# Kernel tuning notes

Hardware: AMD Instinct MI355X
Metric: run time of the kernel (lower is better)

The kernel has to match this reference:

```python
import jax, jax.numpy as jnp
import numpy as np

D_MODEL = 2048
NUM_HEADS = 32
NUM_KV_HEADS = 8
DIM_HEAD = D_MODEL // NUM_HEADS  # 64
REPS = NUM_HEADS // NUM_KV_HEADS  # 4
B, T = 2, 2048


def setup_inputs() -> dict:
    key = jax.random.key(0)
    k_x, k_q, k_k, k_v, k_o = jax.random.split(key, 5)
    s = 1.0 / np.sqrt(D_MODEL)
    return {
        "x": jax.random.normal(k_x, (B, T, D_MODEL), dtype=jnp.float32),
        "wq": jax.random.normal(k_q, (D_MODEL, NUM_HEADS * DIM_HEAD), dtype=jnp.float32) * s,
        "wk": jax.random.normal(k_k, (D_MODEL, NUM_KV_HEADS * DIM_HEAD), dtype=jnp.float32) * s,
        "wv": jax.random.normal(k_v, (D_MODEL, NUM_KV_HEADS * DIM_HEAD), dtype=jnp.float32) * s,
        "wo": jax.random.normal(k_o, (D_MODEL, D_MODEL), dtype=jnp.float32) * s,
    }


def reference(x, wq, wk, wv, wo):
    Bb, Tt, _ = x.shape
    q = (x @ wq).reshape(Bb, Tt, NUM_HEADS, DIM_HEAD)       # [B,T,H,dh]
    k = (x @ wk).reshape(Bb, Tt, NUM_KV_HEADS, DIM_HEAD)    # [B,T,Hkv,dh]
    v = (x @ wv).reshape(Bb, Tt, NUM_KV_HEADS, DIM_HEAD)
    # repeat_interleave KV heads to match Q heads
    k = jnp.repeat(k, REPS, axis=2)                          # [B,T,H,dh]
    v = jnp.repeat(v, REPS, axis=2)
    scale = 1.0 / np.sqrt(DIM_HEAD).astype(np.float32)
    scores = jnp.einsum('bqhd,bkhd->bhqk', q, k) * scale     # [B,H,T,T]
    causal = jnp.tril(jnp.ones((Tt, Tt), dtype=bool))
    scores = jnp.where(causal, scores, -jnp.inf)
    attn = jax.nn.softmax(scores, axis=-1)
    out = jnp.einsum('bhqk,bkhd->bqhd', attn, v)             # [B,T,H,dh]
    out = out.reshape(Bb, Tt, NUM_HEADS * DIM_HEAD)
    return out @ wo
```

## Files before the change

kernel.cpp:

```cpp
#include <hip/hip_runtime.h>

typedef unsigned short u16;
typedef unsigned int u32;
typedef unsigned long long u64;

typedef __bf16 bf16x8 __attribute__((ext_vector_type(8)));
typedef float f32x4 __attribute__((ext_vector_type(4)));
typedef float f32x16 __attribute__((ext_vector_type(16)));
typedef u16 u16x4 __attribute__((ext_vector_type(4)));
typedef u32 u32x4v __attribute__((ext_vector_type(4)));

__device__ __forceinline__ u16 f2bf(float f) {
  u32 u = __builtin_bit_cast(u32, f);
  u += 0x7fffu + ((u >> 16) & 1u);
  return (u16)(u >> 16);
}

__device__ __forceinline__ u32 packbf2(float a, float b) {
  __bf16 x = (__bf16)a, y = (__bf16)b;
  return (u32)__builtin_bit_cast(u16, x) | ((u32)__builtin_bit_cast(u16, y) << 16);
}

__device__ __forceinline__ float fexp2(float x) {
#if __has_builtin(__builtin_amdgcn_exp2f)
  return __builtin_amdgcn_exp2f(x);
#else
  return exp2f(x);
#endif
}

__device__ __forceinline__ void gload_lds16(const void* g, void* lds) {
  __builtin_amdgcn_global_load_lds(
      (const __attribute__((address_space(1))) void*)g,
      (__attribute__((address_space(3))) void*)lds, 16, 0, 0);
}

#define QSCALE 0.18033688011112043f

__global__ __launch_bounds__(256) void prep_kernel(
    const float* __restrict__ x, u16* __restrict__ xb,
    const float* __restrict__ wq, const float* __restrict__ wk,
    const float* __restrict__ wv, const float* __restrict__ wo,
    u16* __restrict__ wqT, u16* __restrict__ wkT,
    u16* __restrict__ wvT, u16* __restrict__ woT) {
  __shared__ float tile[32][33];
  int bid = blockIdx.x;
  if (bid < 8192) {
    int i = (bid * 256 + threadIdx.x) * 4;
    float4 v = *reinterpret_cast<const float4*>(x + i);
    u16x4 o;
    o[0] = f2bf(v.x); o[1] = f2bf(v.y); o[2] = f2bf(v.z); o[3] = f2bf(v.w);
    *reinterpret_cast<u16x4*>(xb + i) = o;
    return;
  }
  bid -= 8192;
  constexpr int K = 2048;
  const float* w_;
  u16* wt;
  int N;
  switch (bid >> 12) {
    case 0: w_ = wq; wt = wqT; N = 2048; break;
    case 1: w_ = wo; wt = woT; N = 2048; break;
    case 2: w_ = wk; wt = wkT; N = 512; break;
    default: w_ = wv; wt = wvT; N = 512; break;
  }
  int rem = bid & 4095;
  int bx = (rem & 63) * 32;
  if (bx >= N) return;
  int by = (rem >> 6) * 32;
  int tx = threadIdx.x & 31, ty = threadIdx.x >> 5;
#pragma unroll
  for (int i = 0; i < 32; i += 8)
    tile[ty + i][tx] = w_[(size_t)(by + ty + i) * N + bx + tx];
  __syncthreads();
#pragma unroll
  for (int i = 0; i < 32; i += 8)
    wt[(size_t)(bx + ty + i) * K + by + tx] = f2bf(tile[tx][ty + i]);
}

__global__ __launch_bounds__(512, 1) void gemm_qkv(
    const u16* __restrict__ A, const u16* __restrict__ BT,
    u16* __restrict__ Cb, u16* __restrict__ Cb2, u16* __restrict__ Cb3) {
  constexpr int K = 2048, NT = 32;
  __shared__ __align__(16) u16 Ab[2][256 * 64];
  __shared__ __align__(16) u16 Bb[2][192 * 64];
  const int t = threadIdx.x;
  const int lane = t & 63;
  const int w = t >> 6;
  const int wm = w >> 2, wn = w & 3;
  const int l15 = lane & 15, l4 = lane >> 4;

  const int nwg = gridDim.x * gridDim.y;
  const int bid = blockIdx.y * gridDim.x + blockIdx.x;
  const int wg = (bid & 7) * (nwg >> 3) + (bid >> 3);
  const int brow = (wg / gridDim.x) * 256;
  const int bcol = (wg % gridDim.x) * 192;

  const int r0 = t >> 3;
  const int gc = ((t & 7) ^ (r0 & 7)) * 8;
  auto stageA = [&](int q, int h, int kt) {
    const u16* src = A + (size_t)(brow + h * 128 + r0) * K + kt * 64 + gc;
    u16* dst = &Ab[q][(h * 128 + r0) * 64 + (t & 7) * 8];
    gload_lds16(src, dst);
    gload_lds16(src + (size_t)64 * K, dst + 64 * 64);
  };
  auto stageB = [&](int q, int c, int kt) {
    const u16* src = BT + (size_t)(bcol + c * 64 + r0) * K + kt * 64 + gc;
    u16* dst = &Bb[q][(c * 64 + r0) * 64 + (t & 7) * 8];
    gload_lds16(src, dst);
  };

  f32x4 acc[8][3];
#pragma unroll
  for (int mi = 0; mi < 8; mi++)
#pragma unroll
    for (int n = 0; n < 3; n++)
#pragma unroll
      for (int r = 0; r < 4; r++) acc[mi][n][r] = 0.f;

  stageA(0, 0, 0); stageA(0, 1, 0);
  stageB(0, 0, 0); stageB(0, 1, 0); stageB(0, 2, 0);
  stageA(1, 0, 1); stageA(1, 1, 1);
  asm volatile("s_waitcnt vmcnt(4)" ::: "memory");
  __builtin_amdgcn_sched_barrier(0);
  __builtin_amdgcn_s_barrier();

  for (int kt = 0; kt < NT; ++kt) {
    const int q = kt & 1;
    const u16* Al = Ab[q];
    const u16* Bl = Bb[q];
    bf16x8 af[8][2], bf[3][2];

#pragma unroll
    for (int m = 0; m < 4; ++m) {
      int row = wm * 128 + m * 16 + l15;
#pragma unroll
      for (int ks = 0; ks < 2; ++ks)
        af[m][ks] = *reinterpret_cast<const bf16x8*>(
            &Al[row * 64 + (((ks * 4 + l4) ^ (row & 7)) * 8)]);
    }
#pragma unroll
    for (int n = 0; n < 3; ++n) {
      int row = wn * 48 + n * 16 + l15;
#pragma unroll
      for (int ks = 0; ks < 2; ++ks)
        bf[n][ks] = *reinterpret_cast<const bf16x8*>(
            &Bl[row * 64 + (((ks * 4 + l4) ^ (row & 7)) * 8)]);
    }
    if (kt + 1 < NT) stageB(q ^ 1, 0, kt + 1);
    __builtin_amdgcn_s_barrier();
    __builtin_amdgcn_s_setprio(1);
#pragma unroll
    for (int ks = 0; ks < 2; ++ks)
#pragma unroll
      for (int m = 0; m < 4; ++m)
#pragma unroll
        for (int n = 0; n < 2; ++n)
          acc[m][n] = __builtin_amdgcn_mfma_f32_16x16x32_bf16(
              af[m][ks], bf[n][ks], acc[m][n], 0, 0, 0);
    __builtin_amdgcn_s_setprio(0);
    __builtin_amdgcn_s_barrier();

#pragma unroll
    for (int m = 4; m < 8; ++m) {
      int row = wm * 128 + m * 16 + l15;
#pragma unroll
      for (int ks = 0; ks < 2; ++ks)
        af[m][ks] = *reinterpret_cast<const bf16x8*>(
            &Al[row * 64 + (((ks * 4 + l4) ^ (row & 7)) * 8)]);
    }
    if (kt + 1 < NT) { stageB(q ^ 1, 1, kt + 1); stageB(q ^ 1, 2, kt + 1); }
    __builtin_amdgcn_s_barrier();
    __builtin_amdgcn_s_setprio(1);
#pragma unroll
    for (int ks = 0; ks < 2; ++ks)
#pragma unroll
      for (int m = 0; m < 4; ++m)
        acc[m][2] = __builtin_amdgcn_mfma_f32_16x16x32_bf16(
            af[m][ks], bf[2][ks], acc[m][2], 0, 0, 0);
    __builtin_amdgcn_s_setprio(0);
    __builtin_amdgcn_s_barrier();

    if (kt + 2 < NT) stageA(q, 0, kt + 2);
    __builtin_amdgcn_s_barrier();
    __builtin_amdgcn_s_setprio(1);
#pragma unroll
    for (int ks = 0; ks < 2; ++ks)
#pragma unroll
      for (int m = 4; m < 8; ++m)
#pragma unroll
        for (int n = 0; n < 2; ++n)
          acc[m][n] = __builtin_amdgcn_mfma_f32_16x16x32_bf16(
              af[m][ks], bf[n][ks], acc[m][n], 0, 0, 0);
    __builtin_amdgcn_s_setprio(0);
    __builtin_amdgcn_s_barrier();

    if (kt + 2 < NT) stageA(q, 1, kt + 2);
    __builtin_amdgcn_s_barrier();
    __builtin_amdgcn_s_setprio(1);
#pragma unroll
    for (int ks = 0; ks < 2; ++ks)
#pragma unroll
      for (int m = 4; m < 8; ++m)
        acc[m][2] = __builtin_amdgcn_mfma_f32_16x16x32_bf16(
            af[m][ks], bf[2][ks], acc[m][2], 0, 0, 0);
    __builtin_amdgcn_s_setprio(0);
    if (kt + 2 < NT) {
      asm volatile("s_waitcnt vmcnt(4)" ::: "memory");
    } else {
      asm volatile("s_waitcnt vmcnt(0)" ::: "memory");
    }
    __builtin_amdgcn_sched_barrier(0);
    __builtin_amdgcn_s_barrier();
  }

#pragma unroll
  for (int mi = 0; mi < 8; ++mi) {
    int grow0 = brow + wm * 128 + mi * 16 + l4 * 4;
#pragma unroll
    for (int n = 0; n < 3; ++n) {
      int gbase = bcol + wn * 48 + n * 16;
      int gcol = gbase + l15;
      if (gbase < 2048) {
#pragma unroll
        for (int r = 0; r < 4; ++r)
          Cb[(size_t)(grow0 + r) * 2048 + gcol] = f2bf(acc[mi][n][r] * QSCALE);
      } else if (gbase < 2560) {
#pragma unroll
        for (int r = 0; r < 4; ++r)
          Cb2[(size_t)(grow0 + r) * 512 + (gcol - 2048)] = f2bf(acc[mi][n][r]);
      } else {
        int col = gcol - 2560;
        int bb = grow0 >> 11, tt = grow0 & 2047;
        u64 wv = (u64)packbf2(acc[mi][n][0], acc[mi][n][1]) |
                 ((u64)packbf2(acc[mi][n][2], acc[mi][n][3]) << 32);
        *reinterpret_cast<u64*>(&Cb3[((size_t)(bb * 512 + col)) * 2048 + tt]) = wv;
      }
    }
  }
}

__global__ __launch_bounds__(512, 2) void gemm256n(
    const u16* __restrict__ A, const u16* __restrict__ BT,
    float* __restrict__ Cf, int M, int N) {
  constexpr int K = 2048, NT = 32;
  __shared__ __align__(16) u16 Ab[2][256 * 64];
  __shared__ __align__(16) u16 Bb[2][128 * 64];
  const int t = threadIdx.x;
  const int lane = t & 63;
  const int w = t >> 6;
  const int wm = w >> 1, wn = w & 1;
  const int l15 = lane & 15, l4 = lane >> 4;

  const int nwg = gridDim.x * gridDim.y;
  const int bid = blockIdx.y * gridDim.x + blockIdx.x;
  const int wg = (bid & 7) * (nwg >> 3) + (bid >> 3);
  const int brow = (wg / gridDim.x) * 256;
  const int bcol = (wg % gridDim.x) * 128;

  const int r0 = t >> 3;
  const int gc = ((t & 7) ^ (r0 & 7)) * 8;
  auto stageA = [&](int q, int h, int kt) {
    const u16* src = A + (size_t)(brow + h * 128 + r0) * K + kt * 64 + gc;
    u16* dst = &Ab[q][(h * 128 + r0) * 64 + (t & 7) * 8];
    gload_lds16(src, dst);
    gload_lds16(src + (size_t)64 * K, dst + 64 * 64);
  };
  auto stageB = [&](int q, int h, int kt) {
    const u16* src = BT + (size_t)(bcol + h * 64 + r0) * K + kt * 64 + gc;
    u16* dst = &Bb[q][(h * 64 + r0) * 64 + (t & 7) * 8];
    gload_lds16(src, dst);
  };

  f32x4 acc[4][4];
#pragma unroll
  for (int m = 0; m < 4; m++)
#pragma unroll
    for (int n = 0; n < 4; n++)
#pragma unroll
      for (int r = 0; r < 4; r++) acc[m][n][r] = 0.f;

  stageA(0, 0, 0); stageA(0, 1, 0);
  stageB(0, 0, 0); stageB(0, 1, 0);
  stageA(1, 0, 1); stageA(1, 1, 1);
  asm volatile("s_waitcnt vmcnt(4)" ::: "memory");
  __builtin_amdgcn_sched_barrier(0);
  __builtin_amdgcn_s_barrier();

  for (int kt = 0; kt < NT; ++kt) {
    const int q = kt & 1;
    const u16* Al = Ab[q];
    const u16* Bl = Bb[q];
    bf16x8 af[4][2], bf[4][2];

#pragma unroll
    for (int m = 0; m < 2; ++m) {
      int row = wm * 64 + m * 16 + l15;
#pragma unroll
      for (int ks = 0; ks < 2; ++ks)
        af[m][ks] = *reinterpret_cast<const bf16x8*>(
            &Al[row * 64 + (((ks * 4 + l4) ^ (row & 7)) * 8)]);
    }
#pragma unroll
    for (int n = 0; n < 2; ++n) {
      int row = wn * 64 + n * 16 + l15;
#pragma unroll
      for (int ks = 0; ks < 2; ++ks)
        bf[n][ks] = *reinterpret_cast<const bf16x8*>(
            &Bl[row * 64 + (((ks * 4 + l4) ^ (row & 7)) * 8)]);
    }
    if (kt + 1 < NT) stageB(q ^ 1, 0, kt + 1);
    __builtin_amdgcn_s_barrier();
    __builtin_amdgcn_s_setprio(1);
#pragma unroll
    for (int ks = 0; ks < 2; ++ks)
#pragma unroll
      for (int m = 0; m < 2; ++m)
#pragma unroll
        for (int n = 0; n < 2; ++n)
          acc[m][n] = __builtin_amdgcn_mfma_f32_16x16x32_bf16(
              af[m][ks], bf[n][ks], acc[m][n], 0, 0, 0);
    __builtin_amdgcn_s_setprio(0);
    __builtin_amdgcn_s_barrier();

#pragma unroll
    for (int m = 2; m < 4; ++m) {
      int row = wm * 64 + m * 16 + l15;
#pragma unroll
      for (int ks = 0; ks < 2; ++ks)
        af[m][ks] = *reinterpret_cast<const bf16x8*>(
            &Al[row * 64 + (((ks * 4 + l4) ^ (row & 7)) * 8)]);
    }
#pragma unroll
    for (int n = 2; n < 4; ++n) {
      int row = wn * 64 + n * 16 + l15;
#pragma unroll
      for (int ks = 0; ks < 2; ++ks)
        bf[n][ks] = *reinterpret_cast<const bf16x8*>(
            &Bl[row * 64 + (((ks * 4 + l4) ^ (row & 7)) * 8)]);
    }
    if (kt + 1 < NT) stageB(q ^ 1, 1, kt + 1);
    __builtin_amdgcn_s_barrier();
    __builtin_amdgcn_s_setprio(1);
#pragma unroll
    for (int ks = 0; ks < 2; ++ks)
#pragma unroll
      for (int m = 0; m < 2; ++m)
#pragma unroll
        for (int n = 2; n < 4; ++n)
          acc[m][n] = __builtin_amdgcn_mfma_f32_16x16x32_bf16(
              af[m][ks], bf[n][ks], acc[m][n], 0, 0, 0);
    __builtin_amdgcn_s_setprio(0);
    __builtin_amdgcn_s_barrier();

    if (kt + 2 < NT) stageA(q, 0, kt + 2);
    __builtin_amdgcn_s_barrier();
    __builtin_amdgcn_s_setprio(1);
#pragma unroll
    for (int ks = 0; ks < 2; ++ks)
#pragma unroll
      for (int m = 2; m < 4; ++m)
#pragma unroll
        for (int n = 0; n < 2; ++n)
          acc[m][n] = __builtin_amdgcn_mfma_f32_16x16x32_bf16(
              af[m][ks], bf[n][ks], acc[m][n], 0, 0, 0);
    __builtin_amdgcn_s_setprio(0);
    __builtin_amdgcn_s_barrier();

    if (kt + 2 < NT) stageA(q, 1, kt + 2);
    __builtin_amdgcn_s_barrier();
    __builtin_amdgcn_s_setprio(1);
#pragma unroll
    for (int ks = 0; ks < 2; ++ks)
#pragma unroll
      for (int m = 2; m < 4; ++m)
#pragma unroll
        for (int n = 2; n < 4; ++n)
          acc[m][n] = __builtin_amdgcn_mfma_f32_16x16x32_bf16(
              af[m][ks], bf[n][ks], acc[m][n], 0, 0, 0);
    __builtin_amdgcn_s_setprio(0);
    if (kt + 2 < NT) {
      asm volatile("s_waitcnt vmcnt(4)" ::: "memory");
    } else {
      asm volatile("s_waitcnt vmcnt(0)" ::: "memory");
    }
    __builtin_amdgcn_sched_barrier(0);
    __builtin_amdgcn_s_barrier();
  }

#pragma unroll
  for (int m = 0; m < 4; ++m) {
    int grow0 = brow + wm * 64 + m * 16 + l4 * 4;
#pragma unroll
    for (int n = 0; n < 4; ++n) {
      int gcol = bcol + wn * 64 + n * 16 + l15;
#pragma unroll
      for (int r = 0; r < 4; ++r)
        Cf[(size_t)(grow0 + r) * N + gcol] = acc[m][n][r];
    }
  }
}

__global__ __launch_bounds__(256, 2) void attn_kernel(
    const u16* __restrict__ Qb, const u16* __restrict__ Kb,
    const u16* __restrict__ VT, u16* __restrict__ Ob) {
  const int bx = blockIdx.x;
  const int kvh = bx & 7;
  const int u = bx >> 3;
  const int jj = u & 7;
  const int v = u >> 3;
  const int h = kvh * 4 + (v & 3);
  const int b = v >> 2;
  const int t = threadIdx.x;
  const int lane = t & 63;
  const int w = t >> 6;
  const int q31 = lane & 31;
  const int hi = lane >> 5;

  __shared__ __align__(16) u16 Ks[2][64 * 64];
  __shared__ __align__(16) u16 Vs[2][64 * 64];
  __shared__ __align__(16) u32 Po[4][32 * 32];

  const size_t Krow0 = (size_t)b * 2048;
  const size_t Vrow0 = ((size_t)b * 8 + kvh) * 64;

  u16* const dk0 = &Ks[0][t * 8];
  u16* const dk1 = &Ks[1][t * 8];
  u16* const dv0 = &Vs[0][t * 8];
  u16* const dv1 = &Vs[1][t * 8];
  const int row0 = t >> 3;
  const int gcs = ((t & 7) ^ (row0 & 7)) * 8;
  const u16* const pk0 = Kb + (Krow0 + row0) * 512 + kvh * 64 + gcs;
  const u16* const pv0 = VT + (Vrow0 + row0) * 2048 + gcs;
  const u16* kp = pk0;
  const u16* vp = pv0;

  auto stage = [&](int buf, const u16* kpp, const u16* vpp) {
    u16* dk = buf ? dk1 : dk0;
    u16* dv = buf ? dv1 : dv0;
    gload_lds16(kpp, dk);
    gload_lds16(kpp + 32 * 512, dk + 2048);
    gload_lds16(vpp, dv);
    gload_lds16(vpp + 32 * 2048, dv + 2048);
  };

  const int swk = (q31 & 7);
  const int nA = 2 * (15 - jj) + 2;
  const int nsteps = 34;

  stage(0, kp, vp);
  __syncthreads();
  int cur = 0;
  int ss = 0;

#pragma unroll
  for (int ph = 0; ph < 2; ++ph) {
    const int qt = ph ? jj : 15 - jj;
    const int nkv = 2 * qt + 2;
    const int wq0 = qt * 128 + w * 32;
    const int mylast = (wq0 + 31) >> 6;

    bf16x8 qf[4];
    {
      const u16* q0 = &Qb[((size_t)b * 2048 + wq0 + q31) * 2048 + h * 64 + hi * 8];
      qf[0] = *reinterpret_cast<const bf16x8*>(q0);
      qf[1] = *reinterpret_cast<const bf16x8*>(q0 + 16);
      qf[2] = *reinterpret_cast<const bf16x8*>(q0 + 32);
      qf[3] = *reinterpret_cast<const bf16x8*>(q0 + 48);
    }

    f32x16 oo0, oo1;
#pragma unroll
    for (int r = 0; r < 16; ++r) { oo0[r] = 0.f; oo1[r] = 0.f; }
    float mr = -1e30f, lr = 0.f;

    for (int kv = 0; kv < nkv; ++kv, ++ss) {
      const int kvbase = kv << 6;
      if (ss + 1 < nsteps) {
        if (ss + 1 == nA) {
          kp = pk0;
          vp = pv0;
        } else {
          kp += 64 * 512;
          vp += 64;
        }
        stage(cur ^ 1, kp, vp);
      }

      if (kv <= mylast) {
        f32x16 s0, s1;
#pragma unroll
        for (int r = 0; r < 16; ++r) { s0[r] = 0.f; s1[r] = 0.f; }
        __builtin_amdgcn_s_setprio(1);
#pragma unroll
        for (int kc = 0; kc < 4; ++kc) {
          const int kcol = ((kc * 2 + hi) ^ swk) * 8;
          bf16x8 kb0 = *reinterpret_cast<const bf16x8*>(&Ks[cur][q31 * 64 + kcol]);
          bf16x8 kb1 = *reinterpret_cast<const bf16x8*>(&Ks[cur][(32 + q31) * 64 + kcol]);
          s0 = __builtin_amdgcn_mfma_f32_32x32x16_bf16(kb0, qf[kc], s0, 0, 0, 0);
          s1 = __builtin_amdgcn_mfma_f32_32x32x16_bf16(kb1, qf[kc], s1, 0, 0, 0);
        }
        __builtin_amdgcn_s_setprio(0);

        if (kvbase + 63 > wq0) {
          const int qg = wq0 + q31;
#pragma unroll
          for (int r = 0; r < 16; ++r) {
            int crow = ((r >> 2) << 3) + (r & 3) + 4 * hi;
            if (kvbase + crow > qg) s0[r] = -1e30f;
            if (kvbase + 32 + crow > qg) s1[r] = -1e30f;
          }
        }

        float mt[8];
#pragma unroll
        for (int r = 0; r < 8; ++r)
          mt[r] = fmaxf(fmaxf(s0[r], s0[r + 8]), fmaxf(s1[r], s1[r + 8]));
#pragma unroll
        for (int st = 4; st; st >>= 1)
#pragma unroll
          for (int r = 0; r < 8; ++r)
            if (r < st) mt[r] = fmaxf(mt[r], mt[r + st]);
        float mx = fmaxf(mt[0], __shfl_xor(mt[0], 32));
        if (!__all(mx <= mr + 8.f)) {
          float mnew = fmaxf(mr, mx);
          float alpha = fexp2(mr - mnew);
          lr *= alpha;
#pragma unroll
          for (int r = 0; r < 16; ++r) { oo0[r] *= alpha; oo1[r] *= alpha; }
          mr = mnew;
        }
        float st_[8];
#pragma unroll
        for (int r = 0; r < 16; ++r) {
          s0[r] = fexp2(s0[r] - mr);
          s1[r] = fexp2(s1[r] - mr);
        }
#pragma unroll
        for (int r = 0; r < 8; ++r)
          st_[r] = (s0[r] + s0[r + 8]) + (s1[r] + s1[r + 8]);
#pragma unroll
        for (int stp = 4; stp; stp >>= 1)
#pragma unroll
          for (int r = 0; r < 8; ++r)
            if (r < stp) st_[r] += st_[r + stp];
        float rs = st_[0] + __shfl_xor(st_[0], 32);
        lr += rs;

        u32 W0[4][2], W1[4][2];
#pragma unroll
        for (int rr = 0; rr < 4; ++rr)
#pragma unroll
          for (int sx = 0; sx < 2; ++sx) {
            W0[rr][sx] = packbf2(s0[4 * rr + 2 * sx], s0[4 * rr + 2 * sx + 1]);
            W1[rr][sx] = packbf2(s1[4 * rr + 2 * sx], s1[4 * rr + 2 * sx + 1]);
          }
        bf16x8 pb[4];
#pragma unroll
        for (int cc = 0; cc < 2; ++cc) {
          const int rrA = 2 * cc, rrB = 2 * cc + 1;
          {
            u32 z0 = hi ? W0[rrA][0] : W0[rrB][0];
            u32 z1 = hi ? W0[rrA][1] : W0[rrB][1];
            u32 z0x = (u32)__shfl_xor((int)z0, 32);
            u32 z1x = (u32)__shfl_xor((int)z1, 32);
            u32x4v pv4 = {hi ? z0x : W0[rrA][0], hi ? z1x : W0[rrA][1],
                          hi ? W0[rrB][0] : z0x, hi ? W0[rrB][1] : z1x};
            pb[cc] = __builtin_bit_cast(bf16x8, pv4);
          }
          {
            u32 z0 = hi ? W1[rrA][0] : W1[rrB][0];
            u32 z1 = hi ? W1[rrA][1] : W1[rrB][1];
            u32 z0x = (u32)__shfl_xor((int)z0, 32);
            u32 z1x = (u32)__shfl_xor((int)z1, 32);
            u32x4v pv4 = {hi ? z0x : W1[rrA][0], hi ? z1x : W1[rrA][1],
                          hi ? W1[rrB][0] : z0x, hi ? W1[rrB][1] : z1x};
            pb[2 + cc] = __builtin_bit_cast(bf16x8, pv4);
          }
        }

        __builtin_amdgcn_s_setprio(1);
#pragma unroll
        for (int kc2 = 0; kc2 < 4; ++kc2) {
          const int vcol = ((kc2 * 2 + hi) ^ swk) * 8;
          bf16x8 va0 = *reinterpret_cast<const bf16x8*>(&Vs[cur][q31 * 64 + vcol]);
          bf16x8 va1 = *reinterpret_cast<const bf16x8*>(&Vs[cur][(32 + q31) * 64 + vcol]);
          oo0 = __builtin_amdgcn_mfma_f32_32x32x16_bf16(va0, pb[kc2], oo0, 0, 0, 0);
          oo1 = __builtin_amdgcn_mfma_f32_32x32x16_bf16(va1, pb[kc2], oo1, 0, 0, 0);
        }
        __builtin_amdgcn_s_setprio(0);
      }

      __syncthreads();
      cur ^= 1;
    }

    {
      float rcp = 1.0f / lr;
      u32* po = &Po[w][0];
      const int swq = (q31 & 7) << 2;
#pragma unroll
      for (int rr = 0; rr < 4; ++rr) {
        u64 w0 = (u64)packbf2(oo0[4 * rr] * rcp, oo0[4 * rr + 1] * rcp) |
                 ((u64)packbf2(oo0[4 * rr + 2] * rcp, oo0[4 * rr + 3] * rcp) << 32);
        *reinterpret_cast<u64*>(&po[q31 * 32 + ((4 * rr + 2 * hi) ^ swq)]) = w0;
        u64 w1 = (u64)packbf2(oo1[4 * rr] * rcp, oo1[4 * rr + 1] * rcp) |
                 ((u64)packbf2(oo1[4 * rr + 2] * rcp, oo1[4 * rr + 3] * rcp) << 32);
        *reinterpret_cast<u64*>(&po[q31 * 32 + ((16 + 4 * rr + 2 * hi) ^ swq)]) = w1;
      }
      const int qq = lane >> 1, hf = lane & 1;
      const int swr = (qq & 7) << 2;
      u32* og = (u32*)Ob + ((size_t)b * 2048 + wq0 + qq) * 1024 + h * 32 + hf * 16;
#pragma unroll
      for (int j = 0; j < 4; ++j) {
        uint4 d = *reinterpret_cast<const uint4*>(
            &po[qq * 32 + ((hf * 16 + j * 4) ^ swr)]);
        *reinterpret_cast<uint4*>(&og[j * 4]) = d;
      }
    }
    __syncthreads();
  }
}

extern "C" void kernel_launch(void* const* d_in, const int* in_sizes, int n_in,
                              void* d_out, int out_size, void* d_ws, size_t ws_size,
                              hipStream_t stream) {
  const float* x = (const float*)d_in[0];
  const float* wq = (const float*)d_in[1];
  const float* wk = (const float*)d_in[2];
  const float* wv = (const float*)d_in[3];
  const float* wo = (const float*)d_in[4];
  float* out = (float*)d_out;

  char* p = (char*)d_ws;
  u16* xb = (u16*)p;   p += (size_t)4096 * 2048 * 2;
  u16* wqT = (u16*)p;  p += (size_t)2048 * 2048 * 2;
  u16* wkT = (u16*)p;  p += (size_t)512 * 2048 * 2;
  u16* wvT = (u16*)p;  p += (size_t)512 * 2048 * 2;
  u16* woT = (u16*)p;  p += (size_t)2048 * 2048 * 2;
  u16* Qb = (u16*)p;   p += (size_t)4096 * 2048 * 2;
  u16* Kb = (u16*)p;   p += (size_t)4096 * 512 * 2;
  u16* VTb = (u16*)p;  p += (size_t)2 * 512 * 2048 * 2;
  u16* attn = xb;

  prep_kernel<<<8192 + 16384, 256, 0, stream>>>(
      x, xb, wq, wk, wv, wo, wqT, wkT, wvT, woT);

  gemm_qkv<<<dim3(16, 16), 512, 0, stream>>>(xb, wqT, Qb, Kb, VTb);

  attn_kernel<<<512, 256, 0, stream>>>(Qb, Kb, VTb, attn);

  gemm256n<<<dim3(2048 / 128, 4096 / 256), 512, 0, stream>>>(
      attn, woT, out, 4096, 2048);
}
```

Measured before the change: 184.2 us.

## Load K/V fragments directly from global memory instead of LDS double-buffering

Removes the shared-memory double-buffered K/V staging and block-wide barriers. Each wave now loads its K and V MFMA operands straight from global memory into registers and loops only up to its own causal limit. This drops LDS traffic and barrier stalls, and lets waves with less causal work finish early. In exchange, the four waves no longer share K/V tiles through LDS, so global/L2 load traffic rises about fourfold and there is no explicit prefetch to hide load latency.

After: 237.6 us. 29.0% more time.

```diff
diff --git a/kernel.cpp b/kernel.cpp
--- a/kernel.cpp
+++ b/kernel.cpp
@@ -417,46 +417,19 @@
   const int q31 = lane & 31;
   const int hi = lane >> 5;
 
-  __shared__ __align__(16) u16 Ks[2][64 * 64];
-  __shared__ __align__(16) u16 Vs[2][64 * 64];
   __shared__ __align__(16) u32 Po[4][32 * 32];
 
   const size_t Krow0 = (size_t)b * 2048;
   const size_t Vrow0 = ((size_t)b * 8 + kvh) * 64;
 
-  u16* const dk0 = &Ks[0][t * 8];
-  u16* const dk1 = &Ks[1][t * 8];
-  u16* const dv0 = &Vs[0][t * 8];
-  u16* const dv1 = &Vs[1][t * 8];
-  const int row0 = t >> 3;
-  const int gcs = ((t & 7) ^ (row0 & 7)) * 8;
-  const u16* const pk0 = Kb + (Krow0 + row0) * 512 + kvh * 64 + gcs;
-  const u16* const pv0 = VT + (Vrow0 + row0) * 2048 + gcs;
-  const u16* kp = pk0;
-  const u16* vp = pv0;
-
-  auto stage = [&](int buf, const u16* kpp, const u16* vpp) {
-    u16* dk = buf ? dk1 : dk0;
-    u16* dv = buf ? dv1 : dv0;
-    gload_lds16(kpp, dk);
-    gload_lds16(kpp + 32 * 512, dk + 2048);
-    gload_lds16(vpp, dv);
-    gload_lds16(vpp + 32 * 2048, dv + 2048);
-  };
-
-  const int swk = (q31 & 7);
-  const int nA = 2 * (15 - jj) + 2;
-  const int nsteps = 34;
-
-  stage(0, kp, vp);
-  __syncthreads();
-  int cur = 0;
-  int ss = 0;
+  const u16* const kb0 = Kb + (Krow0 + q31) * 512 + kvh * 64 + hi * 8;
+  const u16* const kb1 = kb0 + 32 * 512;
+  const u16* const vb0 = VT + (Vrow0 + q31) * 2048 + hi * 8;
+  const u16* const vb1 = vb0 + 32 * 2048;
 
 #pragma unroll
   for (int ph = 0; ph < 2; ++ph) {
     const int qt = ph ? jj : 15 - jj;
-    const int nkv = 2 * qt + 2;
     const int wq0 = qt * 128 + w * 32;
     const int mylast = (wq0 + 31) >> 6;
 
@@ -474,125 +447,126 @@
     for (int r = 0; r < 16; ++r) { oo0[r] = 0.f; oo1[r] = 0.f; }
     float mr = -1e30f, lr = 0.f;
 
-    for (int kv = 0; kv < nkv; ++kv, ++ss) {
+    const u16* kA = kb0;
+    const u16* kB = kb1;
+    const u16* vA = vb0;
+    const u16* vB = vb1;
+
+    for (int kv = 0; kv <= mylast; ++kv) {
       const int kvbase = kv << 6;
-      if (ss + 1 < nsteps) {
-        if (ss + 1 == nA) {
-          kp = pk0;
-          vp = pv0;
-        } else {
-          kp += 64 * 512;
-          vp += 64;
+
+      bf16x8 kf0[4], kf1[4];
+#pragma unroll
+      for (int kc = 0; kc < 4; ++kc) {
+        kf0[kc] = *reinterpret_cast<const bf16x8*>(kA + kc * 16);
+        kf1[kc] = *reinterpret_cast<const bf16x8*>(kB + kc * 16);
+      }
+
+      f32x16 s0, s1;
+#pragma unroll
+      for (int r = 0; r < 16; ++r) { s0[r] = 0.f; s1[r] = 0.f; }
+      __builtin_amdgcn_s_setprio(1);
+#pragma unroll
+      for (int kc = 0; kc < 4; ++kc) {
+        s0 = __builtin_amdgcn_mfma_f32_32x32x16_bf16(kf0[kc], qf[kc], s0, 0, 0, 0);
+        s1 = __builtin_amdgcn_mfma_f32_32x32x16_bf16(kf1[kc], qf[kc], s1, 0, 0, 0);
+      }
+      __builtin_amdgcn_s_setprio(0);
+
+      bf16x8 vf0[4], vf1[4];
+#pragma unroll
+      for (int kc = 0; kc < 4; ++kc) {
+        vf0[kc] = *reinterpret_cast<const bf16x8*>(vA + kc * 16);
+        vf1[kc] = *reinterpret_cast<const bf16x8*>(vB + kc * 16);
+      }
+
+      if (kvbase + 63 > wq0) {
+        const int qg = wq0 + q31;
+#pragma unroll
+        for (int r = 0; r < 16; ++r) {
+          int crow = ((r >> 2) << 3) + (r & 3) + 4 * hi;
+          if (kvbase + crow > qg) s0[r] = -1e30f;
+          if (kvbase + 32 + crow > qg) s1[r] = -1e30f;
         }
-        stage(cur ^ 1, kp, vp);
-      }
-
-      if (kv <= mylast) {
-        f32x16 s0, s1;
-#pragma unroll
-        for (int r = 0; r < 16; ++r) { s0[r] = 0.f; s1[r] = 0.f; }
-        __builtin_amdgcn_s_setprio(1);
-#pragma unroll
-        for (int kc = 0; kc < 4; ++kc) {
-          const int kcol = ((kc * 2 + hi) ^ swk) * 8;
-          bf16x8 kb0 = *reinterpret_cast<const bf16x8*>(&Ks[cur][q31 * 64 + kcol]);
-          bf16x8 kb1 = *reinterpret_cast<const bf16x8*>(&Ks[cur][(32 + q31) * 64 + kcol]);
-          s0 = __builtin_amdgcn_mfma_f32_32x32x16_bf16(kb0, qf[kc], s0, 0, 0, 0);
-          s1 = __builtin_amdgcn_mfma_f32_32x32x16_bf16(kb1, qf[kc], s1, 0, 0, 0);
+      }
+
+      float mt[8];
+#pragma unroll
+      for (int r = 0; r < 8; ++r)
+        mt[r] = fmaxf(fmaxf(s0[r], s0[r + 8]), fmaxf(s1[r], s1[r + 8]));
+#pragma unroll
+      for (int st = 4; st; st >>= 1)
+#pragma unroll
+        for (int r = 0; r < 8; ++r)
+          if (r < st) mt[r] = fmaxf(mt[r], mt[r + st]);
+      float mx = fmaxf(mt[0], __shfl_xor(mt[0], 32));
+      if (!__all(mx <= mr + 8.f)) {
+        float mnew = fmaxf(mr, mx);
+        float alpha = fexp2(mr - mnew);
+        lr *= alpha;
+#pragma unroll
+        for (int r = 0; r < 16; ++r) { oo0[r] *= alpha; oo1[r] *= alpha; }
+        mr = mnew;
+      }
+      float st_[8];
+#pragma unroll
+      for (int r = 0; r < 16; ++r) {
+        s0[r] = fexp2(s0[r] - mr);
+        s1[r] = fexp2(s1[r] - mr);
+      }
+#pragma unroll
+      for (int r = 0; r < 8; ++r)
+        st_[r] = (s0[r] + s0[r + 8]) + (s1[r] + s1[r + 8]);
+#pragma unroll
+      for (int stp = 4; stp; stp >>= 1)
+#pragma unroll
+        for (int r = 0; r < 8; ++r)
+          if (r < stp) st_[r] += st_[r + stp];
+      float rs = st_[0] + __shfl_xor(st_[0], 32);
+      lr += rs;
+
+      u32 W0[4][2], W1[4][2];
+#pragma unroll
+      for (int rr = 0; rr < 4; ++rr)
+#pragma unroll
+        for (int sx = 0; sx < 2; ++sx) {
+          W0[rr][sx] = packbf2(s0[4 * rr + 2 * sx], s0[4 * rr + 2 * sx + 1]);
+          W1[rr][sx] = packbf2(s1[4 * rr + 2 * sx], s1[4 * rr + 2 * sx + 1]);
         }
-        __builtin_amdgcn_s_setprio(0);
-
-        if (kvbase + 63 > wq0) {
-          const int qg = wq0 + q31;
-#pragma unroll
-          for (int r = 0; r < 16; ++r) {
-            int crow = ((r >> 2) << 3) + (r & 3) + 4 * hi;
-            if (kvbase + crow > qg) s0[r] = -1e30f;
-            if (kvbase + 32 + crow > qg) s1[r] = -1e30f;
-          }
+      bf16x8 pb[4];
+#pragma unroll
+      for (int cc = 0; cc < 2; ++cc) {
+        const int rrA = 2 * cc, rrB = 2 * cc + 1;
+        {
+          u32 z0 = hi ? W0[rrA][0] : W0[rrB][0];
+          u32 z1 = hi ? W0[rrA][1] : W0[rrB][1];
+          u32 z0x = (u32)__shfl_xor((int)z0, 32);
+          u32 z1x = (u32)__shfl_xor((int)z1, 32);
+          u32x4v pv4 = {hi ? z0x : W0[rrA][0], hi ? z1x : W0[rrA][1],
+                        hi ? W0[rrB][0] : z0x, hi ? W0[rrB][1] : z1x};
+          pb[cc] = __builtin_bit_cast(bf16x8, pv4);
         }
-
-        float mt[8];
-#pragma unroll
-        for (int r = 0; r < 8; ++r)
-          mt[r] = fmaxf(fmaxf(s0[r], s0[r + 8]), fmaxf(s1[r], s1[r + 8]));
-#pragma unroll
-        for (int st = 4; st; st >>= 1)
-#pragma unroll
-          for (int r = 0; r < 8; ++r)
-            if (r < st) mt[r] = fmaxf(mt[r], mt[r + st]);
-        float mx = fmaxf(mt[0], __shfl_xor(mt[0], 32));
-        if (!__all(mx <= mr + 8.f)) {
-          float mnew = fmaxf(mr, mx);
-          float alpha = fexp2(mr - mnew);
-          lr *= alpha;
-#pragma unroll
-          for (int r = 0; r < 16; ++r) { oo0[r] *= alpha; oo1[r] *= alpha; }
-          mr = mnew;
+        {
+          u32 z0 = hi ? W1[rrA][0] : W1[rrB][0];
+          u32 z1 = hi ? W1[rrA][1] : W1[rrB][1];
+          u32 z0x = (u32)__shfl_xor((int)z0, 32);
+          u32 z1x = (u32)__shfl_xor((int)z1, 32);
+          u32x4v pv4 = {hi ? z0x : W1[rrA][0], hi ? z1x : W1[rrA][1],
+                        hi ? W1[rrB][0] : z0x, hi ? W1[rrB][1] : z1x};
+          pb[2 + cc] = __builtin_bit_cast(bf16x8, pv4);
         }
-        float st_[8];
-#pragma unroll
-        for (int r = 0; r < 16; ++r) {
-          s0[r] = fexp2(s0[r] - mr);
-          s1[r] = fexp2(s1[r] - mr);
-        }
-#pragma unroll
-        for (int r = 0; r < 8; ++r)
-          st_[r] = (s0[r] + s0[r + 8]) + (s1[r] + s1[r + 8]);
-#pragma unroll
-        for (int stp = 4; stp; stp >>= 1)
-#pragma unroll
-          for (int r = 0; r < 8; ++r)
-            if (r < stp) st_[r] += st_[r + stp];
-        float rs = st_[0] + __shfl_xor(st_[0], 32);
-        lr += rs;
-
-        u32 W0[4][2], W1[4][2];
-#pragma unroll
-        for (int rr = 0; rr < 4; ++rr)
-#pragma unroll
-          for (int sx = 0; sx < 2; ++sx) {
-            W0[rr][sx] = packbf2(s0[4 * rr + 2 * sx], s0[4 * rr + 2 * sx + 1]);
-            W1[rr][sx] = packbf2(s1[4 * rr + 2 * sx], s1[4 * rr + 2 * sx + 1]);
-          }
-        bf16x8 pb[4];
-#pragma unroll
-        for (int cc = 0; cc < 2; ++cc) {
-          const int rrA = 2 * cc, rrB = 2 * cc + 1;
-          {
-            u32 z0 = hi ? W0[rrA][0] : W0[rrB][0];
-            u32 z1 = hi ? W0[rrA][1] : W0[rrB][1];
-            u32 z0x = (u32)__shfl_xor((int)z0, 32);
-            u32 z1x = (u32)__shfl_xor((int)z1, 32);
-            u32x4v pv4 = {hi ? z0x : W0[rrA][0], hi ? z1x : W0[rrA][1],
-                          hi ? W0[rrB][0] : z0x, hi ? W0[rrB][1] : z1x};
-            pb[cc] = __builtin_bit_cast(bf16x8, pv4);
-          }
-          {
-            u32 z0 = hi ? W1[rrA][0] : W1[rrB][0];
-            u32 z1 = hi ? W1[rrA][1] : W1[rrB][1];
-            u32 z0x = (u32)__shfl_xor((int)z0, 32);
-            u32 z1x = (u32)__shfl_xor((int)z1, 32);
-            u32x4v pv4 = {hi ? z0x : W1[rrA][0], hi ? z1x : W1[rrA][1],
-                          hi ? W1[rrB][0] : z0x, hi ? W1[rrB][1] : z1x};
-            pb[2 + cc] = __builtin_bit_cast(bf16x8, pv4);
-          }
-        }
-
-        __builtin_amdgcn_s_setprio(1);
-#pragma unroll
-        for (int kc2 = 0; kc2 < 4; ++kc2) {
-          const int vcol = ((kc2 * 2 + hi) ^ swk) * 8;
-          bf16x8 va0 = *reinterpret_cast<const bf16x8*>(&Vs[cur][q31 * 64 + vcol]);
-          bf16x8 va1 = *reinterpret_cast<const bf16x8*>(&Vs[cur][(32 + q31) * 64 + vcol]);
-          oo0 = __builtin_amdgcn_mfma_f32_32x32x16_bf16(va0, pb[kc2], oo0, 0, 0, 0);
-          oo1 = __builtin_amdgcn_mfma_f32_32x32x16_bf16(va1, pb[kc2], oo1, 0, 0, 0);
-        }
-        __builtin_amdgcn_s_setprio(0);
-      }
-
-      __syncthreads();
-      cur ^= 1;
+      }
+
+      __builtin_amdgcn_s_setprio(1);
+#pragma unroll
+      for (int kc2 = 0; kc2 < 4; ++kc2) {
+        oo0 = __builtin_amdgcn_mfma_f32_32x32x16_bf16(vf0[kc2], pb[kc2], oo0, 0, 0, 0);
+        oo1 = __builtin_amdgcn_mfma_f32_32x32x16_bf16(vf1[kc2], pb[kc2], oo1, 0, 0, 0);
+      }
+      __builtin_amdgcn_s_setprio(0);
+
+      kA += 64 * 512; kB += 64 * 512;
+      vA += 64; vB += 64;
     }
 
     {
@@ -618,7 +592,6 @@
         *reinterpret_cast<uint4*>(&og[j * 4]) = d;
       }
     }
-    __syncthreads();
   }
 }
 
```

## Move wo transpose into attention kernel tail and compact prep grid

Applied to the files above, without the earlier changes.

The wo fp32-to-bf16 transpose leaves the prep kernel and runs as extra blocks appended to the attention launch, so it can fill CUs left idle by the 512 attention blocks. The prep grid is compacted so no early-exit blocks are launched for the narrow wk/wv matrices. The attention kernel now uses a single 48KB shared buffer aliased between the two roles, and its launch bound is raised to 3 blocks per CU. Risks are that transpose blocks may be scheduled ahead of attention blocks and delay them, and that the tighter register budget may cause spills in attention.

New measurement: 179.9 us (median of 2 runs). 1.02x faster.

```diff
diff --git a/kernel.cpp b/kernel.cpp
--- a/kernel.cpp
+++ b/kernel.cpp
@@ -40,9 +40,8 @@
 __global__ __launch_bounds__(256) void prep_kernel(
     const float* __restrict__ x, u16* __restrict__ xb,
     const float* __restrict__ wq, const float* __restrict__ wk,
-    const float* __restrict__ wv, const float* __restrict__ wo,
-    u16* __restrict__ wqT, u16* __restrict__ wkT,
-    u16* __restrict__ wvT, u16* __restrict__ woT) {
+    const float* __restrict__ wv,
+    u16* __restrict__ wqT, u16* __restrict__ wkT, u16* __restrict__ wvT) {
   __shared__ float tile[32][33];
   int bid = blockIdx.x;
   if (bid < 8192) {
@@ -57,17 +56,19 @@
   constexpr int K = 2048;
   const float* w_;
   u16* wt;
-  int N;
-  switch (bid >> 12) {
-    case 0: w_ = wq; wt = wqT; N = 2048; break;
-    case 1: w_ = wo; wt = woT; N = 2048; break;
-    case 2: w_ = wk; wt = wkT; N = 512; break;
-    default: w_ = wv; wt = wvT; N = 512; break;
-  }
-  int rem = bid & 4095;
-  int bx = (rem & 63) * 32;
-  if (bx >= N) return;
-  int by = (rem >> 6) * 32;
+  int N, bx, by;
+  if (bid < 4096) {
+    w_ = wq; wt = wqT; N = 2048;
+    bx = (bid & 63) * 32; by = (bid >> 6) * 32;
+  } else if (bid < 5120) {
+    int r = bid - 4096;
+    w_ = wk; wt = wkT; N = 512;
+    bx = (r & 15) * 32; by = (r >> 4) * 32;
+  } else {
+    int r = bid - 5120;
+    w_ = wv; wt = wvT; N = 512;
+    bx = (r & 15) * 32; by = (r >> 4) * 32;
+  }
   int tx = threadIdx.x & 31, ty = threadIdx.x >> 5;
 #pragma unroll
   for (int i = 0; i < 32; i += 8)
@@ -401,10 +402,34 @@
   }
 }
 
-__global__ __launch_bounds__(256, 2) void attn_kernel(
+__global__ __launch_bounds__(256, 3) void attn_wo_kernel(
     const u16* __restrict__ Qb, const u16* __restrict__ Kb,
-    const u16* __restrict__ VT, u16* __restrict__ Ob) {
-  const int bx = blockIdx.x;
+    const u16* __restrict__ VT, u16* __restrict__ Ob,
+    const float* __restrict__ wo, u16* __restrict__ woT) {
+  __shared__ __align__(16) char smem[49152];
+  const int bxall = blockIdx.x;
+
+  if (bxall >= 512) {
+    const int bid = bxall - 512;
+    float(*tile)[33] = reinterpret_cast<float(*)[33]>(smem);
+    int bx = (bid & 63) * 32;
+    int by = (bid >> 6) * 32;
+    int tx = threadIdx.x & 31, ty = threadIdx.x >> 5;
+#pragma unroll
+    for (int i = 0; i < 32; i += 8)
+      tile[ty + i][tx] = wo[(size_t)(by + ty + i) * 2048 + bx + tx];
+    __syncthreads();
+#pragma unroll
+    for (int i = 0; i < 32; i += 8)
+      woT[(size_t)(bx + ty + i) * 2048 + by + tx] = f2bf(tile[tx][ty + i]);
+    return;
+  }
+
+  u16(*Ks)[64 * 64] = reinterpret_cast<u16(*)[64 * 64]>(smem);
+  u16(*Vs)[64 * 64] = reinterpret_cast<u16(*)[64 * 64]>(smem + 16384);
+  u32(*Po)[32 * 32] = reinterpret_cast<u32(*)[32 * 32]>(smem + 32768);
+
+  const int bx = bxall;
   const int kvh = bx & 7;
   const int u = bx >> 3;
   const int jj = u & 7;
@@ -416,10 +441,6 @@
   const int w = t >> 6;
   const int q31 = lane & 31;
   const int hi = lane >> 5;
-
-  __shared__ __align__(16) u16 Ks[2][64 * 64];
-  __shared__ __align__(16) u16 Vs[2][64 * 64];
-  __shared__ __align__(16) u32 Po[4][32 * 32];
 
   const size_t Krow0 = (size_t)b * 2048;
   const size_t Vrow0 = ((size_t)b * 8 + kvh) * 64;
@@ -643,12 +664,12 @@
   u16* VTb = (u16*)p;  p += (size_t)2 * 512 * 2048 * 2;
   u16* attn = xb;
 
-  prep_kernel<<<8192 + 16384, 256, 0, stream>>>(
-      x, xb, wq, wk, wv, wo, wqT, wkT, wvT, woT);
+  prep_kernel<<<14336, 256, 0, stream>>>(
+      x, xb, wq, wk, wv, wqT, wkT, wvT);
 
   gemm_qkv<<<dim3(16, 16), 512, 0, stream>>>(xb, wqT, Qb, Kb, VTb);
 
-  attn_kernel<<<512, 256, 0, stream>>>(Qb, Kb, VTb, attn);
+  attn_wo_kernel<<<512 + 4096, 256, 0, stream>>>(Qb, Kb, VTb, attn, wo, woT);
 
   gemm256n<<<dim3(2048 / 128, 4096 / 256), 512, 0, stream>>>(
       attn, woT, out, 4096, 2048);
```

## Halve attention block size to 64-query tiles and compact prep grid

Applied to the files above, without the earlier changes.

The attention kernel now uses 128-thread blocks (two waves), each handling a pair of 64-row query tiles instead of 128-row tiles, doubling the grid to 1024 blocks and raising target occupancy. With 64-row tiles every KV step is needed, so the per-wave skip check is removed and the mask only applies on the diagonal tile. K/V staging is split into four loads per thread. The prep kernel grid is compacted so it no longer launches the idle blocks for the narrow K/V weights. The trade-off is less K/V reuse per block, since each tile loaded from global memory now serves half as many query rows, plus more blocks to schedule.

New measurement: 189.8 us. 3.0% more time.

```diff
diff --git a/kernel.cpp b/kernel.cpp
--- a/kernel.cpp
+++ b/kernel.cpp
@@ -57,17 +57,23 @@
   constexpr int K = 2048;
   const float* w_;
   u16* wt;
-  int N;
-  switch (bid >> 12) {
-    case 0: w_ = wq; wt = wqT; N = 2048; break;
-    case 1: w_ = wo; wt = woT; N = 2048; break;
-    case 2: w_ = wk; wt = wkT; N = 512; break;
-    default: w_ = wv; wt = wvT; N = 512; break;
+  int N, bx, by;
+  if (bid < 4096) {
+    w_ = wq; wt = wqT; N = 2048;
+    bx = (bid & 63) * 32; by = (bid >> 6) * 32;
+  } else if (bid < 5120) {
+    int r = bid - 4096;
+    w_ = wk; wt = wkT; N = 512;
+    bx = (r & 15) * 32; by = (r >> 4) * 32;
+  } else if (bid < 6144) {
+    int r = bid - 5120;
+    w_ = wv; wt = wvT; N = 512;
+    bx = (r & 15) * 32; by = (r >> 4) * 32;
+  } else {
+    int r = bid - 6144;
+    w_ = wo; wt = woT; N = 2048;
+    bx = (r & 63) * 32; by = (r >> 6) * 32;
   }
-  int rem = bid & 4095;
-  int bx = (rem & 63) * 32;
-  if (bx >= N) return;
-  int by = (rem >> 6) * 32;
   int tx = threadIdx.x & 31, ty = threadIdx.x >> 5;
 #pragma unroll
   for (int i = 0; i < 32; i += 8)
@@ -401,14 +407,14 @@
   }
 }
 
-__global__ __launch_bounds__(256, 2) void attn_kernel(
+__global__ __launch_bounds__(128, 4) void attn_kernel(
     const u16* __restrict__ Qb, const u16* __restrict__ Kb,
     const u16* __restrict__ VT, u16* __restrict__ Ob) {
   const int bx = blockIdx.x;
   const int kvh = bx & 7;
   const int u = bx >> 3;
-  const int jj = u & 7;
-  const int v = u >> 3;
+  const int jj = u & 15;
+  const int v = u >> 4;
   const int h = kvh * 4 + (v & 3);
   const int b = v >> 2;
   const int t = threadIdx.x;
@@ -419,7 +425,7 @@
 
   __shared__ __align__(16) u16 Ks[2][64 * 64];
   __shared__ __align__(16) u16 Vs[2][64 * 64];
-  __shared__ __align__(16) u32 Po[4][32 * 32];
+  __shared__ __align__(16) u32 Po[2][32 * 32];
 
   const size_t Krow0 = (size_t)b * 2048;
   const size_t Vrow0 = ((size_t)b * 8 + kvh) * 64;
@@ -438,14 +444,15 @@
   auto stage = [&](int buf, const u16* kpp, const u16* vpp) {
     u16* dk = buf ? dk1 : dk0;
     u16* dv = buf ? dv1 : dv0;
-    gload_lds16(kpp, dk);
-    gload_lds16(kpp + 32 * 512, dk + 2048);
-    gload_lds16(vpp, dv);
-    gload_lds16(vpp + 32 * 2048, dv + 2048);
+#pragma unroll
+    for (int c = 0; c < 4; ++c) {
+      gload_lds16(kpp + (size_t)c * 16 * 512, dk + c * 1024);
+      gload_lds16(vpp + (size_t)c * 16 * 2048, dv + c * 1024);
+    }
   };
 
   const int swk = (q31 & 7);
-  const int nA = 2 * (15 - jj) + 2;
+  const int nA = 32 - jj;
   const int nsteps = 34;
 
   stage(0, kp, vp);
@@ -455,10 +462,9 @@
 
 #pragma unroll
   for (int ph = 0; ph < 2; ++ph) {
-    const int qt = ph ? jj : 15 - jj;
-    const int nkv = 2 * qt + 2;
-    const int wq0 = qt * 128 + w * 32;
-    const int mylast = (wq0 + 31) >> 6;
+    const int qt = ph ? jj : 31 - jj;
+    const int nkv = qt + 1;
+    const int wq0 = qt * 64 + w * 32;
 
     bf16x8 qf[4];
     {
@@ -475,7 +481,6 @@
     float mr = -1e30f, lr = 0.f;
 
     for (int kv = 0; kv < nkv; ++kv, ++ss) {
-      const int kvbase = kv << 6;
       if (ss + 1 < nsteps) {
         if (ss + 1 == nA) {
           kp = pk0;
@@ -487,109 +492,108 @@
         stage(cur ^ 1, kp, vp);
       }
 
-      if (kv <= mylast) {
-        f32x16 s0, s1;
-#pragma unroll
-        for (int r = 0; r < 16; ++r) { s0[r] = 0.f; s1[r] = 0.f; }
-        __builtin_amdgcn_s_setprio(1);
-#pragma unroll
-        for (int kc = 0; kc < 4; ++kc) {
-          const int kcol = ((kc * 2 + hi) ^ swk) * 8;
-          bf16x8 kb0 = *reinterpret_cast<const bf16x8*>(&Ks[cur][q31 * 64 + kcol]);
-          bf16x8 kb1 = *reinterpret_cast<const bf16x8*>(&Ks[cur][(32 + q31) * 64 + kcol]);
-          s0 = __builtin_amdgcn_mfma_f32_32x32x16_bf16(kb0, qf[kc], s0, 0, 0, 0);
-          s1 = __builtin_amdgcn_mfma_f32_32x32x16_bf16(kb1, qf[kc], s1, 0, 0, 0);
+      f32x16 s0, s1;
+#pragma unroll
+      for (int r = 0; r < 16; ++r) { s0[r] = 0.f; s1[r] = 0.f; }
+      __builtin_amdgcn_s_setprio(1);
+#pragma unroll
+      for (int kc = 0; kc < 4; ++kc) {
+        const int kcol = ((kc * 2 + hi) ^ swk) * 8;
+        bf16x8 kb0 = *reinterpret_cast<const bf16x8*>(&Ks[cur][q31 * 64 + kcol]);
+        bf16x8 kb1 = *reinterpret_cast<const bf16x8*>(&Ks[cur][(32 + q31) * 64 + kcol]);
+        s0 = __builtin_amdgcn_mfma_f32_32x32x16_bf16(kb0, qf[kc], s0, 0, 0, 0);
+        s1 = __builtin_amdgcn_mfma_f32_32x32x16_bf16(kb1, qf[kc], s1, 0, 0, 0);
+      }
+      __builtin_amdgcn_s_setprio(0);
+
+      if (kv == qt) {
+        const int kvbase = qt << 6;
+        const int qg = wq0 + q31;
+#pragma unroll
+        for (int r = 0; r < 16; ++r) {
+          int crow = ((r >> 2) << 3) + (r & 3) + 4 * hi;
+          if (kvbase + crow > qg) s0[r] = -1e30f;
+          if (kvbase + 32 + crow > qg) s1[r] = -1e30f;
         }
-        __builtin_amdgcn_s_setprio(0);
-
-        if (kvbase + 63 > wq0) {
-          const int qg = wq0 + q31;
-#pragma unroll
-          for (int r = 0; r < 16; ++r) {
-            int crow = ((r >> 2) << 3) + (r & 3) + 4 * hi;
-            if (kvbase + crow > qg) s0[r] = -1e30f;
-            if (kvbase + 32 + crow > qg) s1[r] = -1e30f;
-          }
+      }
+
+      float mt[8];
+#pragma unroll
+      for (int r = 0; r < 8; ++r)
+        mt[r] = fmaxf(fmaxf(s0[r], s0[r + 8]), fmaxf(s1[r], s1[r + 8]));
+#pragma unroll
+      for (int st = 4; st; st >>= 1)
+#pragma unroll
+        for (int r = 0; r < 8; ++r)
+          if (r < st) mt[r] = fmaxf(mt[r], mt[r + st]);
+      float mx = fmaxf(mt[0], __shfl_xor(mt[0], 32));
+      if (!__all(mx <= mr + 8.f)) {
+        float mnew = fmaxf(mr, mx);
+        float alpha = fexp2(mr - mnew);
+        lr *= alpha;
+#pragma unroll
+        for (int r = 0; r < 16; ++r) { oo0[r] *= alpha; oo1[r] *= alpha; }
+        mr = mnew;
+      }
+      float st_[8];
+#pragma unroll
+      for (int r = 0; r < 16; ++r) {
+        s0[r] = fexp2(s0[r] - mr);
+        s1[r] = fexp2(s1[r] - mr);
+      }
+#pragma unroll
+      for (int r = 0; r < 8; ++r)
+        st_[r] = (s0[r] + s0[r + 8]) + (s1[r] + s1[r + 8]);
+#pragma unroll
+      for (int stp = 4; stp; stp >>= 1)
+#pragma unroll
+        for (int r = 0; r < 8; ++r)
+          if (r < stp) st_[r] += st_[r + stp];
+      float rs = st_[0] + __shfl_xor(st_[0], 32);
+      lr += rs;
+
+      u32 W0[4][2], W1[4][2];
+#pragma unroll
+      for (int rr = 0; rr < 4; ++rr)
+#pragma unroll
+        for (int sx = 0; sx < 2; ++sx) {
+          W0[rr][sx] = packbf2(s0[4 * rr + 2 * sx], s0[4 * rr + 2 * sx + 1]);
+          W1[rr][sx] = packbf2(s1[4 * rr + 2 * sx], s1[4 * rr + 2 * sx + 1]);
         }
-
-        float mt[8];
-#pragma unroll
-        for (int r = 0; r < 8; ++r)
-          mt[r] = fmaxf(fmaxf(s0[r], s0[r + 8]), fmaxf(s1[r], s1[r + 8]));
-#pragma unroll
-        for (int st = 4; st; st >>= 1)
-#pragma unroll
-          for (int r = 0; r < 8; ++r)
-            if (r < st) mt[r] = fmaxf(mt[r], mt[r + st]);
-        float mx = fmaxf(mt[0], __shfl_xor(mt[0], 32));
-        if (!__all(mx <= mr + 8.f)) {
-          float mnew = fmaxf(mr, mx);
-          float alpha = fexp2(mr - mnew);
-          lr *= alpha;
-#pragma unroll
-          for (int r = 0; r < 16; ++r) { oo0[r] *= alpha; oo1[r] *= alpha; }
-          mr = mnew;
+      bf16x8 pb[4];
+#pragma unroll
+      for (int cc = 0; cc < 2; ++cc) {
+        const int rrA = 2 * cc, rrB = 2 * cc + 1;
+        {
+          u32 z0 = hi ? W0[rrA][0] : W0[rrB][0];
+          u32 z1 = hi ? W0[rrA][1] : W0[rrB][1];
+          u32 z0x = (u32)__shfl_xor((int)z0, 32);
+          u32 z1x = (u32)__shfl_xor((int)z1, 32);
+          u32x4v pv4 = {hi ? z0x : W0[rrA][0], hi ? z1x : W0[rrA][1],
+                        hi ? W0[rrB][0] : z0x, hi ? W0[rrB][1] : z1x};
+          pb[cc] = __builtin_bit_cast(bf16x8, pv4);
         }
-        float st_[8];
-#pragma unroll
-        for (int r = 0; r < 16; ++r) {
-          s0[r] = fexp2(s0[r] - mr);
-          s1[r] = fexp2(s1[r] - mr);
+        {
+          u32 z0 = hi ? W1[rrA][0] : W1[rrB][0];
+          u32 z1 = hi ? W1[rrA][1] : W1[rrB][1];
+          u32 z0x = (u32)__shfl_xor((int)z0, 32);
+          u32 z1x = (u32)__shfl_xor((int)z1, 32);
+          u32x4v pv4 = {hi ? z0x : W1[rrA][0], hi ? z1x : W1[rrA][1],
+                        hi ? W1[rrB][0] : z0x, hi ? W1[rrB][1] : z1x};
+          pb[2 + cc] = __builtin_bit_cast(bf16x8, pv4);
         }
-#pragma unroll
-        for (int r = 0; r < 8; ++r)
-          st_[r] = (s0[r] + s0[r + 8]) + (s1[r] + s1[r + 8]);
-#pragma unroll
-        for (int stp = 4; stp; stp >>= 1)
-#pragma unroll
-          for (int r = 0; r < 8; ++r)
-            if (r < stp) st_[r] += st_[r + stp];
-        float rs = st_[0] + __shfl_xor(st_[0], 32);
-        lr += rs;
-
-        u32 W0[4][2], W1[4][2];
-#pragma unroll
-        for (int rr = 0; rr < 4; ++rr)
-#pragma unroll
-          for (int sx = 0; sx < 2; ++sx) {
-            W0[rr][sx] = packbf2(s0[4 * rr + 2 * sx], s0[4 * rr + 2 * sx + 1]);
-            W1[rr][sx] = packbf2(s1[4 * rr + 2 * sx], s1[4 * rr + 2 * sx + 1]);
-          }
-        bf16x8 pb[4];
-#pragma unroll
-        for (int cc = 0; cc < 2; ++cc) {
-          const int rrA = 2 * cc, rrB = 2 * cc + 1;
-          {
-            u32 z0 = hi ? W0[rrA][0] : W0[rrB][0];
-            u32 z1 = hi ? W0[rrA][1] : W0[rrB][1];
-            u32 z0x = (u32)__shfl_xor((int)z0, 32);
-            u32 z1x = (u32)__shfl_xor((int)z1, 32);
-            u32x4v pv4 = {hi ? z0x : W0[rrA][0], hi ? z1x : W0[rrA][1],
-                          hi ? W0[rrB][0] : z0x, hi ? W0[rrB][1] : z1x};
-            pb[cc] = __builtin_bit_cast(bf16x8, pv4);
-          }
-          {
-            u32 z0 = hi ? W1[rrA][0] : W1[rrB][0];
-            u32 z1 = hi ? W1[rrA][1] : W1[rrB][1];
-            u32 z0x = (u32)__shfl_xor((int)z0, 32);
-            u32 z1x = (u32)__shfl_xor((int)z1, 32);
-            u32x4v pv4 = {hi ? z0x : W1[rrA][0], hi ? z1x : W1[rrA][1],
-                          hi ? W1[rrB][0] : z0x, hi ? W1[rrB][1] : z1x};
-            pb[2 + cc] = __builtin_bit_cast(bf16x8, pv4);
-          }
-        }
-
-        __builtin_amdgcn_s_setprio(1);
-#pragma unroll
-        for (int kc2 = 0; kc2 < 4; ++kc2) {
-          const int vcol = ((kc2 * 2 + hi) ^ swk) * 8;
-          bf16x8 va0 = *reinterpret_cast<const bf16x8*>(&Vs[cur][q31 * 64 + vcol]);
-          bf16x8 va1 = *reinterpret_cast<const bf16x8*>(&Vs[cur][(32 + q31) * 64 + vcol]);
-          oo0 = __builtin_amdgcn_mfma_f32_32x32x16_bf16(va0, pb[kc2], oo0, 0, 0, 0);
-          oo1 = __builtin_amdgcn_mfma_f32_32x32x16_bf16(va1, pb[kc2], oo1, 0, 0, 0);
-        }
-        __builtin_amdgcn_s_setprio(0);
-      }
+      }
+
+      __builtin_amdgcn_s_setprio(1);
+#pragma unroll
+      for (int kc2 = 0; kc2 < 4; ++kc2) {
+        const int vcol = ((kc2 * 2 + hi) ^ swk) * 8;
+        bf16x8 va0 = *reinterpret_cast<const bf16x8*>(&Vs[cur][q31 * 64 + vcol]);
+        bf16x8 va1 = *reinterpret_cast<const bf16x8*>(&Vs[cur][(32 + q31) * 64 + vcol]);
+        oo0 = __builtin_amdgcn_mfma_f32_32x32x16_bf16(va0, pb[kc2], oo0, 0, 0, 0);
+        oo1 = __builtin_amdgcn_mfma_f32_32x32x16_bf16(va1, pb[kc2], oo1, 0, 0, 0);
+      }
+      __builtin_amdgcn_s_setprio(0);
 
       __syncthreads();
       cur ^= 1;
@@ -643,12 +647,12 @@
   u16* VTb = (u16*)p;  p += (size_t)2 * 512 * 2048 * 2;
   u16* attn = xb;
 
-  prep_kernel<<<8192 + 16384, 256, 0, stream>>>(
+  prep_kernel<<<18432, 256, 0, stream>>>(
       x, xb, wq, wk, wv, wo, wqT, wkT, wvT, woT);
 
   gemm_qkv<<<dim3(16, 16), 512, 0, stream>>>(xb, wqT, Qb, Kb, VTb);
 
-  attn_kernel<<<512, 256, 0, stream>>>(Qb, Kb, VTb, attn);
+  attn_kernel<<<1024, 128, 0, stream>>>(Qb, Kb, VTb, attn);
 
   gemm256n<<<dim3(2048 / 128, 4096 / 256), 512, 0, stream>>>(
       attn, woT, out, 4096, 2048);
```
